# Optimization experiments

Measured on AMD Instinct MI355X. Metric: run time of the kernel, lower is better.

Reference implementation:

```python
import jax, jax.numpy as jnp
import numpy as np
import math

D_MODEL = 1024
DIM_K = 1024
DIM_V = 1024
N_HEADS = 16
B, T = 4, 1024


def setup_inputs() -> dict:
    key = jax.random.key(0)
    ks = jax.random.split(key, 12)
    s = 1.0 / math.sqrt(D_MODEL)
    inp = {
        "x": jax.random.normal(ks[0], (B, T, D_MODEL), jnp.float32),
        "mask": jax.random.randint(ks[1], (T, T), 0, 2, jnp.int32),
        "adj": jax.random.normal(ks[2], (T, T), jnp.float32) * 0.1,
        "Wq": jax.random.normal(ks[3], (D_MODEL, DIM_K), jnp.float32) * s,
        "bq": jnp.zeros((DIM_K,), jnp.float32),
        "Wk": jax.random.normal(ks[4], (D_MODEL, DIM_K), jnp.float32) * s,
        "bk": jnp.zeros((DIM_K,), jnp.float32),
        "Wv": jax.random.normal(ks[5], (D_MODEL, DIM_V), jnp.float32) * s,
        "bv": jnp.zeros((DIM_V,), jnp.float32),
        "Wo": jax.random.normal(ks[6], (DIM_V, D_MODEL), jnp.float32) * (1.0 / math.sqrt(DIM_V)),
        "bo": jnp.zeros((D_MODEL,), jnp.float32),
        "alpha": jnp.asarray(0.0, jnp.float32),
        "n_heads": N_HEADS,
    }
    return inp


def reference(x, mask, adj, Wq, bq, Wk, bk, Wv, bv, Wo, bo, alpha, n_heads):
    b, t, d = x.shape
    dim_k = Wq.shape[1]
    dim_v = Wv.shape[1]
    dkh = dim_k // n_heads
    dvh = dim_v // n_heads
    norm_fact = 1.0 / math.sqrt(dim_k)

    # torch .view(-1, B, T, dkh): plain row-major reshape with heads leading
    Q = (x @ Wq + bq).reshape(n_heads, b, t, dkh)
    K = (x @ Wk + bk).reshape(n_heads, b, t, dkh)
    V = (x @ Wv + bv).reshape(n_heads, b, t, dvh)

    # shared score computation [H, B, T, T]
    g_map = jnp.einsum("hbqd,hbkd->hbqk", Q, K) * norm_fact + adj
    l_map = jnp.where(mask == 0, jnp.asarray(-1e9, g_map.dtype), g_map)

    g_att = jax.nn.softmax(g_map, axis=-1)
    l_att = jax.nn.softmax(l_map, axis=-1)

    x_g = jnp.einsum("hbqk,hbkd->hbqd", g_att, V).reshape(b, t, -1)
    x_l = jnp.einsum("hbqk,hbkd->hbqd", l_att, V).reshape(b, t, -1)

    a = jax.nn.sigmoid(alpha)
    x_o = a * x_g + (1.0 - a) * x_l

    # signed sqrt + L2 normalize (norm=True)
    x_o = jnp.sqrt(jax.nn.relu(x_o)) - jnp.sqrt(jax.nn.relu(-x_o))
    x_o = x_o / jnp.maximum(jnp.linalg.norm(x_o, axis=-1, keepdims=True), 1e-12)

    return (x_o @ Wo + bo).reshape(-1, t, d)
```

## Files before the change

### kernel.cpp

```cpp
#include <hip/hip_runtime.h>
#include <hip/hip_bf16.h>


typedef __attribute__((ext_vector_type(8))) short short8;
typedef __attribute__((ext_vector_type(4))) float f32x4;
typedef __attribute__((ext_vector_type(2))) int i32x2;

__device__ __forceinline__ f32x4 mfma16(short8 a, short8 b, f32x4 c) {
  return __builtin_amdgcn_mfma_f32_16x16x32_bf16(a, b, c, 0, 0, 0);
}

__device__ __forceinline__ unsigned short f2b(float f) {
  __hip_bfloat16 h = __float2bfloat16(f);
  return *reinterpret_cast<unsigned short*>(&h);
}

__device__ __forceinline__ unsigned cvtpk(float lo, float hi) {
  unsigned r;
  asm("v_cvt_pk_bf16_f32 %0, %1, %2" : "=v"(r) : "v"(lo), "v"(hi));
  return r;
}

__device__ __forceinline__ float exp2h(float x) {
  float r;
  asm("v_exp_f32 %0, %1" : "=v"(r) : "v"(x));
  return r;
}

__device__ __forceinline__ unsigned ldsoff(const void* p) {
  return (unsigned)(size_t)(const __attribute__((address_space(3))) char*)p;
}

template <int OFF>
__device__ __forceinline__ i32x2 dstr(unsigned addr) {
  i32x2 d;
  asm volatile("ds_read_b64_tr_b16 %0, %1 offset:%c2"
               : "=v"(d) : "v"(addr), "i"(OFF) : "memory");
  return d;
}

__device__ __forceinline__ void gload_lds16(const void* g, void* l) {
  __builtin_amdgcn_global_load_lds(
      (const __attribute__((address_space(1))) void*)g,
      (__attribute__((address_space(3))) void*)l, 16, 0, 0);
}

__global__ __launch_bounds__(256) void k_cast_x(const float* __restrict__ x,
                                                unsigned short* __restrict__ xb) {
  int i = (blockIdx.x * 256 + threadIdx.x) * 8;
  float4 a = *reinterpret_cast<const float4*>(x + i);
  float4 b = *reinterpret_cast<const float4*>(x + i + 4);
  short8 o;
  o[0] = (short)f2b(a.x); o[1] = (short)f2b(a.y);
  o[2] = (short)f2b(a.z); o[3] = (short)f2b(a.w);
  o[4] = (short)f2b(b.x); o[5] = (short)f2b(b.y);
  o[6] = (short)f2b(b.z); o[7] = (short)f2b(b.w);
  *reinterpret_cast<short8*>(xb + i) = o;
}

__global__ __launch_bounds__(256) void k_transW(const float* __restrict__ Wq,
                                                const float* __restrict__ Wk,
                                                const float* __restrict__ Wv,
                                                const float* __restrict__ Wo,
                                                unsigned short* __restrict__ WcatT,
                                                unsigned short* __restrict__ WoT) {
  int wsel = blockIdx.z;
  const float* src = wsel == 0 ? Wq : wsel == 1 ? Wk : wsel == 2 ? Wv : Wo;
  unsigned short* dst = (wsel < 3) ? (WcatT + (size_t)wsel * 1024 * 1024) : WoT;
  int k0 = blockIdx.x * 64, n0 = blockIdx.y * 64;
  __shared__ float tile[64][65];
  int tr = threadIdx.x >> 6, tc = threadIdx.x & 63;
#pragma unroll
  for (int i = 0; i < 16; ++i) {
    int r = i * 4 + tr;
    tile[r][tc] = src[(size_t)(k0 + r) * 1024 + n0 + tc];
  }
  __syncthreads();
#pragma unroll
  for (int i = 0; i < 16; ++i) {
    int r = i * 4 + tr;
    dst[(size_t)(n0 + r) * 1024 + k0 + tc] = f2b(tile[tc][r]);
  }
}

__global__ __launch_bounds__(256) void k_pack(const float* __restrict__ adj,
                                              const int* __restrict__ mask,
                                              unsigned int* __restrict__ AM) {
  const float L2E = 1.4426950408889634f;
  int i = (blockIdx.x * 256 + threadIdx.x) * 4;
  int q = i >> 10, c = i & 1023;
  float4 a = *reinterpret_cast<const float4*>(adj + i);
  int4 m = *reinterpret_cast<const int4*>(mask + i);
  int kt = c >> 6, h = (c >> 5) & 1, g = (c >> 3) & 3, e0 = c & 7;
  unsigned W = (unsigned)((kt * 8 + h * 4 + g) * 8192 + q * 8 + e0);
  uint4 o;
  o.x = ((unsigned)f2b(a.x * L2E) << 16) | (m.x != 0 ? 1u : 0u);
  o.y = ((unsigned)f2b(a.y * L2E) << 16) | (m.y != 0 ? 1u : 0u);
  o.z = ((unsigned)f2b(a.z * L2E) << 16) | (m.z != 0 ? 1u : 0u);
  o.w = ((unsigned)f2b(a.w * L2E) << 16) | (m.w != 0 ? 1u : 0u);
  *reinterpret_cast<uint4*>(AM + W) = o;
}

template <int MODE>
__global__ __launch_bounds__(256) void k_gemm(
    const unsigned short* __restrict__ A, const unsigned short* __restrict__ BT,
    float* __restrict__ outF,
    unsigned short* __restrict__ oQ, unsigned short* __restrict__ oK,
    unsigned short* __restrict__ oV,
    const float* __restrict__ b0, const float* __restrict__ b1,
    const float* __restrict__ b2, int M, int N, int K) {
  __shared__ unsigned short As[128 * 32], Bs[128 * 32];
  const int tid = threadIdx.x;
  const int w = tid >> 6, l = tid & 63, l15 = l & 15, l4 = l >> 4;
  const int m0 = blockIdx.x * 128, n0 = blockIdx.y * 128;
  const int wm = (w >> 1) * 64, wn = (w & 1) * 64;
  f32x4 acc[4][4];
#pragma unroll
  for (int i = 0; i < 4; ++i)
#pragma unroll
    for (int j = 0; j < 4; ++j) acc[i][j] = f32x4{0.f, 0.f, 0.f, 0.f};

  const int nkt = K >> 5;
  for (int kt = 0; kt < nkt; ++kt) {
#pragma unroll
    for (int i = 0; i < 2; ++i) {
      int c = i * 256 + tid;
      gload_lds16(A + (size_t)(m0 + (c >> 2)) * K + kt * 32 + (c & 3) * 8,
                  (char*)As + c * 16);
      gload_lds16(BT + (size_t)(n0 + (c >> 2)) * K + kt * 32 + (c & 3) * 8,
                  (char*)Bs + c * 16);
    }
    __syncthreads();
    short8 af[4], bf[4];
#pragma unroll
    for (int i = 0; i < 4; ++i)
      af[i] = *reinterpret_cast<const short8*>(As + (wm + i * 16 + l15) * 32 + l4 * 8);
#pragma unroll
    for (int j = 0; j < 4; ++j)
      bf[j] = *reinterpret_cast<const short8*>(Bs + (wn + j * 16 + l15) * 32 + l4 * 8);
#pragma unroll
    for (int i = 0; i < 4; ++i)
#pragma unroll
      for (int j = 0; j < 4; ++j) acc[i][j] = mfma16(af[i], bf[j], acc[i][j]);
    __syncthreads();
  }
#pragma unroll
  for (int i = 0; i < 4; ++i)
#pragma unroll
    for (int j = 0; j < 4; ++j) {
      int gr0 = m0 + wm + i * 16 + l4 * 4;
      int gc = n0 + wn + j * 16 + l15;
      if (MODE == 0) {
        int mat = gc >> 10, nl = gc & 1023;
        const float* bp = mat == 0 ? b0 : mat == 1 ? b1 : b2;
        unsigned short* op = mat == 0 ? oQ : mat == 1 ? oK : oV;
        float bb = bp[nl];
#pragma unroll
        for (int r = 0; r < 4; ++r)
          op[(size_t)(gr0 + r) * 1024 + nl] = f2b(acc[i][j][r] + bb);
      } else {
        float bb = b0[gc];
#pragma unroll
        for (int r = 0; r < 4; ++r)
          outF[(size_t)(gr0 + r) * N + gc] = acc[i][j][r] + bb;
      }
    }
}

__global__ __launch_bounds__(256, 4) void k_attn(
    const unsigned short* __restrict__ Qb, const unsigned short* __restrict__ Kb,
    const unsigned short* __restrict__ Vb, const unsigned int* __restrict__ AM,
    float* __restrict__ Xg, float* __restrict__ Xl) {
  const int g = blockIdx.x;
  const int q0 = blockIdx.y * 64;
  const int tid = threadIdx.x;
  const int w = tid >> 6, l = tid & 63, l15 = l & 15, l4 = l >> 4;

  __shared__ unsigned short Kt[2][2][64][32];
  __shared__ unsigned short Vs[2][4][64][16];

  const size_t gbase = (size_t)g << 16;
  const unsigned short* Qg = Qb + gbase;
  const unsigned short* Kg = Kb + gbase;
  const unsigned short* Vg = Vb + gbase;

  short8 qf[2];
  {
    const unsigned short* qp = Qg + (size_t)(q0 + w * 16 + l15) * 64 + l4 * 8;
    qf[0] = *reinterpret_cast<const short8*>(qp);
    qf[1] = *reinterpret_cast<const short8*>(qp + 32);
  }
  short8 onesf;
#pragma unroll
  for (int j = 0; j < 8; ++j) onesf[j] = (short)0x3F80;

  f32x4 accg[4], accl[4];
#pragma unroll
  for (int d = 0; d < 4; ++d) {
    accg[d] = f32x4{0.f, 0.f, 0.f, 0.f};
    accl[d] = f32x4{0.f, 0.f, 0.f, 0.f};
  }
  f32x4 sumg = f32x4{0.f, 0.f, 0.f, 0.f}, suml = f32x4{0.f, 0.f, 0.f, 0.f};

  const float NF2 = 0.04508422002778f;
  const int q_abs = q0 + w * 16 + l15;
  const int qrow = q0 + w * 16 + l4 * 4;

  int koff[4];
#pragma unroll
  for (int cb = 0; cb < 4; ++cb) {
    int key = 8 * (l15 >> 2) + (l15 & 3) + 4 * (cb & 1) + 32 * (cb >> 1);
    int sl = l4 ^ (((key >> 1) ^ (key >> 3)) & 3);
    koff[cb] = key * 64 + sl * 16;
  }
  const unsigned ktb = ldsoff(&Kt[0][0][0][0]);
  const unsigned vsb = ldsoff(&Vs[0][0][0][0]) + (unsigned)(l4 * 256 + l15 * 8);
  const unsigned* AMq = AM + (size_t)q_abs * 8;

  auto stage = [&](int b, int kk0) {
#pragma unroll
    for (int i = 0; i < 2; ++i) {
      int c = i * 256 + tid;
      int dk = c >> 8, key = (c >> 2) & 63, slot = c & 3;
      int ls = slot ^ (((key >> 1) ^ (key >> 3)) & 3);
      gload_lds16(Kg + (size_t)(kk0 + key) * 64 + dk * 32 + ls * 8,
                  (char*)Kt + b * 8192 + c * 16);
    }
#pragma unroll
    for (int i = 0; i < 2; ++i) {
      int c = i * 256 + tid;
      int db = c >> 7, k = (c >> 1) & 63, h = c & 1;
      gload_lds16(Vg + (size_t)(kk0 + k) * 64 + db * 16 + h * 8,
                  (char*)Vs + b * 8192 + c * 16);
    }
  };

  stage(0, 0);
  __syncthreads();

#pragma unroll 2
  for (int kt = 0; kt < 16; ++kt) {
    const int b = kt & 1;
    if (kt < 15) stage(b ^ 1, (kt + 1) * 64);

    union { uint4 v; unsigned u[4]; } amc[4];
    {
      const unsigned* p0 = AMq + (size_t)(kt * 8 + l4) * 8192;
      const unsigned* p1 = AMq + (size_t)(kt * 8 + 4 + l4) * 8192;
      amc[0].v = *reinterpret_cast<const uint4*>(p0);
      amc[1].v = *reinterpret_cast<const uint4*>(p0 + 4);
      amc[2].v = *reinterpret_cast<const uint4*>(p1);
      amc[3].v = *reinterpret_cast<const uint4*>(p1 + 4);
    }

    f32x4 accs[4];
#pragma unroll
    for (int cb = 0; cb < 4; ++cb) {
      accs[cb] = f32x4{0.f, 0.f, 0.f, 0.f};
#pragma unroll
      for (int dk = 0; dk < 2; ++dk) {
        short8 kf = *reinterpret_cast<const short8*>(
            (const char*)Kt + b * 8192 + dk * 4096 + koff[cb]);
        accs[cb] = mfma16(kf, qf[dk], accs[cb]);
      }
    }

    const unsigned vb = vsb + (unsigned)(b << 13);
    union { short8 s8; i32x2 d[2]; } vf[4];
#pragma unroll
    for (int db = 0; db < 4; ++db) {
      vf[db].d[0] = dstr<0>(vb + db * 2048);
      vf[db].d[1] = dstr<128>(vb + db * 2048);
    }

    unsigned pgq[8], plq[8];
#pragma unroll
    for (int cb = 0; cb < 4; ++cb) {
      unsigned a0 = amc[cb].u[0], a1 = amc[cb].u[1];
      unsigned a2 = amc[cb].u[2], a3 = amc[cb].u[3];
      float e0 = exp2h(fmaf(accs[cb][0], NF2, __uint_as_float(a0 & 0xffff0000u)));
      float e1 = exp2h(fmaf(accs[cb][1], NF2, __uint_as_float(a1 & 0xffff0000u)));
      float e2 = exp2h(fmaf(accs[cb][2], NF2, __uint_as_float(a2 & 0xffff0000u)));
      float e3 = exp2h(fmaf(accs[cb][3], NF2, __uint_as_float(a3 & 0xffff0000u)));
      float z0 = (a0 & 1u) ? e0 : 0.f;
      float z1 = (a1 & 1u) ? e1 : 0.f;
      float z2 = (a2 & 1u) ? e2 : 0.f;
      float z3 = (a3 & 1u) ? e3 : 0.f;
      pgq[cb * 2]     = cvtpk(e0, e1);
      pgq[cb * 2 + 1] = cvtpk(e2, e3);
      plq[cb * 2]     = cvtpk(z0, z1);
      plq[cb * 2 + 1] = cvtpk(z2, z3);
    }
    union { short8 s8; unsigned u[4]; } pg0, pl0, pg1, pl1;
#pragma unroll
    for (int v = 0; v < 4; ++v) {
      pg0.u[v] = pgq[v];     pl0.u[v] = plq[v];
      pg1.u[v] = pgq[4 + v]; pl1.u[v] = plq[4 + v];
    }

    asm volatile("s_waitcnt lgkmcnt(0)" ::: "memory");
    __builtin_amdgcn_sched_barrier(0);
#pragma unroll
    for (int db = 0; db < 4; ++db) {
      accg[db] = mfma16(pg0.s8, vf[db].s8, accg[db]);
      accl[db] = mfma16(pl0.s8, vf[db].s8, accl[db]);
    }
    sumg = mfma16(pg0.s8, onesf, sumg);
    suml = mfma16(pl0.s8, onesf, suml);

#pragma unroll
    for (int db = 0; db < 4; ++db) {
      vf[db].d[0] = dstr<1024>(vb + db * 2048);
      vf[db].d[1] = dstr<1024 + 128>(vb + db * 2048);
    }
    asm volatile("s_waitcnt lgkmcnt(0)" ::: "memory");
    __builtin_amdgcn_sched_barrier(0);
#pragma unroll
    for (int db = 0; db < 4; ++db) {
      accg[db] = mfma16(pg1.s8, vf[db].s8, accg[db]);
      accl[db] = mfma16(pl1.s8, vf[db].s8, accl[db]);
    }
    sumg = mfma16(pg1.s8, onesf, sumg);
    suml = mfma16(pl1.s8, onesf, suml);

    __syncthreads();
  }

#pragma unroll
  for (int r = 0; r < 4; ++r) {
    float ig = 1.f / sumg[r];
    float il = suml[r] > 0.f ? 1.f / suml[r] : 0.f;
#pragma unroll
    for (int db = 0; db < 4; ++db) {
      size_t o = gbase + (size_t)(qrow + r) * 64 + db * 16 + l15;
      Xg[o] = accg[db][r] * ig;
      Xl[o] = accl[db][r] * il;
    }
  }
}

__global__ __launch_bounds__(256) void k_combine(const float* __restrict__ Xg,
                                                 const float* __restrict__ Xl,
                                                 const float* __restrict__ alphap,
                                                 unsigned short* __restrict__ xob) {
  int row = blockIdx.x, tid = threadIdx.x;
  int w = tid >> 6, l = tid & 63;
  size_t base = (size_t)row * 1024 + tid * 4;
  float a = 1.f / (1.f + __expf(-alphap[0]));
  float4 gx = *reinterpret_cast<const float4*>(Xg + base);
  float4 lx = *reinterpret_cast<const float4*>(Xl + base);
  float v[4];
  {
    float t0 = a * gx.x + (1.f - a) * lx.x;
    float t1 = a * gx.y + (1.f - a) * lx.y;
    float t2 = a * gx.z + (1.f - a) * lx.z;
    float t3 = a * gx.w + (1.f - a) * lx.w;
    v[0] = t0 >= 0.f ? sqrtf(t0) : -sqrtf(-t0);
    v[1] = t1 >= 0.f ? sqrtf(t1) : -sqrtf(-t1);
    v[2] = t2 >= 0.f ? sqrtf(t2) : -sqrtf(-t2);
    v[3] = t3 >= 0.f ? sqrtf(t3) : -sqrtf(-t3);
  }
  float ss = v[0] * v[0] + v[1] * v[1] + v[2] * v[2] + v[3] * v[3];
#pragma unroll
  for (int off = 1; off < 64; off <<= 1) ss += __shfl_xor(ss, off);
  __shared__ float wsum[4];
  if (l == 0) wsum[w] = ss;
  __syncthreads();
  float tot = wsum[0] + wsum[1] + wsum[2] + wsum[3];
  float scale = 1.f / fmaxf(sqrtf(tot), 1e-12f);
  ushort4 o;
  o.x = f2b(v[0] * scale); o.y = f2b(v[1] * scale);
  o.z = f2b(v[2] * scale); o.w = f2b(v[3] * scale);
  *reinterpret_cast<ushort4*>(xob + base) = o;
}

extern "C" void kernel_launch(void* const* d_in, const int* in_sizes, int n_in,
                              void* d_out, int out_size, void* d_ws, size_t ws_size,
                              hipStream_t stream) {
  const float* x     = (const float*)d_in[0];
  const int*   mask  = (const int*)d_in[1];
  const float* adj   = (const float*)d_in[2];
  const float* Wq    = (const float*)d_in[3];
  const float* bq    = (const float*)d_in[4];
  const float* Wk    = (const float*)d_in[5];
  const float* bk    = (const float*)d_in[6];
  const float* Wv    = (const float*)d_in[7];
  const float* bv    = (const float*)d_in[8];
  const float* Wo    = (const float*)d_in[9];
  const float* bo    = (const float*)d_in[10];
  const float* alpha = (const float*)d_in[11];
  float* out = (float*)d_out;
  char* ws = (char*)d_ws;

  unsigned short* xb    = (unsigned short*)(ws + 0);
  unsigned short* WcatT = (unsigned short*)(ws + 8388608);
  unsigned short* WoT   = (unsigned short*)(ws + 14680064);
  unsigned short* Qb    = (unsigned short*)(ws + 16777216);
  unsigned short* Kb    = (unsigned short*)(ws + 25165824);
  unsigned short* Vb    = (unsigned short*)(ws + 33554432);
  float*          Xg    = (float*)(ws + 41943040);
  float*          Xl    = (float*)(ws + 58720256);
  unsigned short* xob   = (unsigned short*)(ws + 75497472);
  unsigned int*   AM    = (unsigned int*)(ws + 83886080);

  k_cast_x<<<2048, 256, 0, stream>>>(x, xb);
  k_transW<<<dim3(16, 16, 4), 256, 0, stream>>>(Wq, Wk, Wv, Wo, WcatT, WoT);
  k_pack<<<1024, 256, 0, stream>>>(adj, mask, AM);
  k_gemm<0><<<dim3(32, 24), 256, 0, stream>>>(xb, WcatT, nullptr, Qb, Kb, Vb,
                                              bq, bk, bv, 4096, 3072, 1024);
  k_attn<<<dim3(64, 16), 256, 0, stream>>>(Qb, Kb, Vb, AM, Xg, Xl);
  k_combine<<<4096, 256, 0, stream>>>(Xg, Xl, alpha, xob);
  k_gemm<1><<<dim3(32, 8), 256, 0, stream>>>(xob, WoT, out, nullptr, nullptr,
                                             nullptr, bo, bo, bo, 4096, 1024, 1024);
}
```

Baseline: 230.5 us.

## Fuse alpha blend into attention epilogue, double-buffer GEMM LDS, prioritize MFMA waves

The attention kernel now applies the sigmoid(alpha) weights in its epilogue and writes a single blended output. This replaces the separate global and local buffers, roughly halving the intermediate write and read traffic that feeds the combine kernel. The GEMM kernel double-buffers its LDS tiles so the next K-tile load is issued while the current tile is being multiplied, at the cost of twice the shared memory per block. s_setprio brackets around the MFMA sections of the attention loop try to favour matrix-core issue over other waves.

```diff
diff --git a/kernel.cpp b/kernel.cpp
--- a/kernel.cpp
+++ b/kernel.cpp
@@ -109,7 +109,7 @@
     unsigned short* __restrict__ oV,
     const float* __restrict__ b0, const float* __restrict__ b1,
     const float* __restrict__ b2, int M, int N, int K) {
-  __shared__ unsigned short As[128 * 32], Bs[128 * 32];
+  __shared__ unsigned short As[2][128 * 32], Bs[2][128 * 32];
   const int tid = threadIdx.x;
   const int w = tid >> 6, l = tid & 63, l15 = l & 15, l4 = l >> 4;
   const int m0 = blockIdx.x * 128, n0 = blockIdx.y * 128;
@@ -120,24 +120,31 @@
 #pragma unroll
     for (int j = 0; j < 4; ++j) acc[i][j] = f32x4{0.f, 0.f, 0.f, 0.f};
 
-  const int nkt = K >> 5;
-  for (int kt = 0; kt < nkt; ++kt) {
+  auto stage = [&](int b, int kt) {
 #pragma unroll
     for (int i = 0; i < 2; ++i) {
       int c = i * 256 + tid;
       gload_lds16(A + (size_t)(m0 + (c >> 2)) * K + kt * 32 + (c & 3) * 8,
-                  (char*)As + c * 16);
+                  (char*)As[b] + c * 16);
       gload_lds16(BT + (size_t)(n0 + (c >> 2)) * K + kt * 32 + (c & 3) * 8,
-                  (char*)Bs + c * 16);
-    }
-    __syncthreads();
+                  (char*)Bs[b] + c * 16);
+    }
+  };
+
+  const int nkt = K >> 5;
+  stage(0, 0);
+  __syncthreads();
+
+  for (int kt = 0; kt < nkt; ++kt) {
+    const int b = kt & 1;
+    if (kt + 1 < nkt) stage(b ^ 1, kt + 1);
     short8 af[4], bf[4];
 #pragma unroll
     for (int i = 0; i < 4; ++i)
-      af[i] = *reinterpret_cast<const short8*>(As + (wm + i * 16 + l15) * 32 + l4 * 8);
+      af[i] = *reinterpret_cast<const short8*>(As[b] + (wm + i * 16 + l15) * 32 + l4 * 8);
 #pragma unroll
     for (int j = 0; j < 4; ++j)
-      bf[j] = *reinterpret_cast<const short8*>(Bs + (wn + j * 16 + l15) * 32 + l4 * 8);
+      bf[j] = *reinterpret_cast<const short8*>(Bs[b] + (wn + j * 16 + l15) * 32 + l4 * 8);
 #pragma unroll
     for (int i = 0; i < 4; ++i)
 #pragma unroll
@@ -170,7 +177,7 @@
 __global__ __launch_bounds__(256, 4) void k_attn(
     const unsigned short* __restrict__ Qb, const unsigned short* __restrict__ Kb,
     const unsigned short* __restrict__ Vb, const unsigned int* __restrict__ AM,
-    float* __restrict__ Xg, float* __restrict__ Xl) {
+    const float* __restrict__ alphap, float* __restrict__ Xc) {
   const int g = blockIdx.x;
   const int q0 = blockIdx.y * 64;
   const int tid = threadIdx.x;
@@ -213,7 +220,6 @@
     int sl = l4 ^ (((key >> 1) ^ (key >> 3)) & 3);
     koff[cb] = key * 64 + sl * 16;
   }
-  const unsigned ktb = ldsoff(&Kt[0][0][0][0]);
   const unsigned vsb = ldsoff(&Vs[0][0][0][0]) + (unsigned)(l4 * 256 + l15 * 8);
   const unsigned* AMq = AM + (size_t)q_abs * 8;
 
@@ -254,6 +260,7 @@
     }
 
     f32x4 accs[4];
+    __builtin_amdgcn_s_setprio(1);
 #pragma unroll
     for (int cb = 0; cb < 4; ++cb) {
       accs[cb] = f32x4{0.f, 0.f, 0.f, 0.f};
@@ -264,6 +271,7 @@
         accs[cb] = mfma16(kf, qf[dk], accs[cb]);
       }
     }
+    __builtin_amdgcn_s_setprio(0);
 
     const unsigned vb = vsb + (unsigned)(b << 13);
     union { short8 s8; i32x2 d[2]; } vf[4];
@@ -300,6 +308,7 @@
 
     asm volatile("s_waitcnt lgkmcnt(0)" ::: "memory");
     __builtin_amdgcn_sched_barrier(0);
+    __builtin_amdgcn_s_setprio(1);
 #pragma unroll
     for (int db = 0; db < 4; ++db) {
       accg[db] = mfma16(pg0.s8, vf[db].s8, accg[db]);
@@ -307,6 +316,7 @@
     }
     sumg = mfma16(pg0.s8, onesf, sumg);
     suml = mfma16(pl0.s8, onesf, suml);
+    __builtin_amdgcn_s_setprio(0);
 
 #pragma unroll
     for (int db = 0; db < 4; ++db) {
@@ -315,6 +325,7 @@
     }
     asm volatile("s_waitcnt lgkmcnt(0)" ::: "memory");
     __builtin_amdgcn_sched_barrier(0);
+    __builtin_amdgcn_s_setprio(1);
 #pragma unroll
     for (int db = 0; db < 4; ++db) {
       accg[db] = mfma16(pg1.s8, vf[db].s8, accg[db]);
@@ -322,44 +333,35 @@
     }
     sumg = mfma16(pg1.s8, onesf, sumg);
     suml = mfma16(pl1.s8, onesf, suml);
+    __builtin_amdgcn_s_setprio(0);
 
     __syncthreads();
   }
 
+  const float a = 1.f / (1.f + __expf(-alphap[0]));
 #pragma unroll
   for (int r = 0; r < 4; ++r) {
-    float ig = 1.f / sumg[r];
-    float il = suml[r] > 0.f ? 1.f / suml[r] : 0.f;
+    float ig = a / sumg[r];
+    float il = suml[r] > 0.f ? (1.f - a) / suml[r] : 0.f;
 #pragma unroll
     for (int db = 0; db < 4; ++db) {
       size_t o = gbase + (size_t)(qrow + r) * 64 + db * 16 + l15;
-      Xg[o] = accg[db][r] * ig;
-      Xl[o] = accl[db][r] * il;
-    }
-  }
-}
-
-__global__ __launch_bounds__(256) void k_combine(const float* __restrict__ Xg,
-                                                 const float* __restrict__ Xl,
-                                                 const float* __restrict__ alphap,
+      Xc[o] = accg[db][r] * ig + accl[db][r] * il;
+    }
+  }
+}
+
+__global__ __launch_bounds__(256) void k_combine(const float* __restrict__ Xc,
                                                  unsigned short* __restrict__ xob) {
   int row = blockIdx.x, tid = threadIdx.x;
   int w = tid >> 6, l = tid & 63;
   size_t base = (size_t)row * 1024 + tid * 4;
-  float a = 1.f / (1.f + __expf(-alphap[0]));
-  float4 gx = *reinterpret_cast<const float4*>(Xg + base);
-  float4 lx = *reinterpret_cast<const float4*>(Xl + base);
+  float4 cx = *reinterpret_cast<const float4*>(Xc + base);
   float v[4];
-  {
-    float t0 = a * gx.x + (1.f - a) * lx.x;
-    float t1 = a * gx.y + (1.f - a) * lx.y;
-    float t2 = a * gx.z + (1.f - a) * lx.z;
-    float t3 = a * gx.w + (1.f - a) * lx.w;
-    v[0] = t0 >= 0.f ? sqrtf(t0) : -sqrtf(-t0);
-    v[1] = t1 >= 0.f ? sqrtf(t1) : -sqrtf(-t1);
-    v[2] = t2 >= 0.f ? sqrtf(t2) : -sqrtf(-t2);
-    v[3] = t3 >= 0.f ? sqrtf(t3) : -sqrtf(-t3);
-  }
+  v[0] = cx.x >= 0.f ? sqrtf(cx.x) : -sqrtf(-cx.x);
+  v[1] = cx.y >= 0.f ? sqrtf(cx.y) : -sqrtf(-cx.y);
+  v[2] = cx.z >= 0.f ? sqrtf(cx.z) : -sqrtf(-cx.z);
+  v[3] = cx.w >= 0.f ? sqrtf(cx.w) : -sqrtf(-cx.w);
   float ss = v[0] * v[0] + v[1] * v[1] + v[2] * v[2] + v[3] * v[3];
 #pragma unroll
   for (int off = 1; off < 64; off <<= 1) ss += __shfl_xor(ss, off);
@@ -398,18 +400,17 @@
   unsigned short* Qb    = (unsigned short*)(ws + 16777216);
   unsigned short* Kb    = (unsigned short*)(ws + 25165824);
   unsigned short* Vb    = (unsigned short*)(ws + 33554432);
-  float*          Xg    = (float*)(ws + 41943040);
-  float*          Xl    = (float*)(ws + 58720256);
-  unsigned short* xob   = (unsigned short*)(ws + 75497472);
-  unsigned int*   AM    = (unsigned int*)(ws + 83886080);
+  float*          Xc    = (float*)(ws + 41943040);
+  unsigned short* xob   = (unsigned short*)(ws + 58720256);
+  unsigned int*   AM    = (unsigned int*)(ws + 67108864);
 
   k_cast_x<<<2048, 256, 0, stream>>>(x, xb);
   k_transW<<<dim3(16, 16, 4), 256, 0, stream>>>(Wq, Wk, Wv, Wo, WcatT, WoT);
   k_pack<<<1024, 256, 0, stream>>>(adj, mask, AM);
   k_gemm<0><<<dim3(32, 24), 256, 0, stream>>>(xb, WcatT, nullptr, Qb, Kb, Vb,
                                               bq, bk, bv, 4096, 3072, 1024);
-  k_attn<<<dim3(64, 16), 256, 0, stream>>>(Qb, Kb, Vb, AM, Xg, Xl);
-  k_combine<<<4096, 256, 0, stream>>>(Xg, Xl, alpha, xob);
+  k_attn<<<dim3(64, 16), 256, 0, stream>>>(Qb, Kb, Vb, AM, alpha, Xc);
+  k_combine<<<4096, 256, 0, stream>>>(Xc, xob);
   k_gemm<1><<<dim3(32, 8), 256, 0, stream>>>(xob, WoT, out, nullptr, nullptr,
                                              nullptr, bo, bo, bo, 4096, 1024, 1024);
 }
```

Result: faster. 222.8 us (-3.3%).
